# Kernel tuning notes

Hardware: AMD Instinct MI355X
Metric: run time of the kernel (lower is better)

Reference implementation:

```python
import jax, jax.numpy as jnp
import numpy as np

J = 24  # fixed pooling window (SampleLength/N = 1200/50)


def setup_inputs() -> dict:
    key = jax.random.key(0)
    k1, k2, k3 = jax.random.split(key, 3)
    T, N, K, C = 786432, 50, 400, 10  # T = 32768 segments * J
    x = jax.random.normal(k1, (T, N), dtype=jnp.float32)
    W1 = jax.random.normal(k2, (K, N), dtype=jnp.float32) * 0.1
    W2 = jax.random.normal(k3, (C, K), dtype=jnp.float32) * 0.1
    return {"x": x, "W1": W1, "W2": W2}


def reference(x, W1, W2):
    # linear + relu: [T, N] @ [N, K] -> [T, K]
    local_features = jax.nn.relu(jnp.einsum('tn,kn->tk', x, W1))
    # fixed-window mean over consecutive J rows: [T, K] -> [T//J, K]
    T, K = local_features.shape
    features = local_features.reshape(T // J, J, K).mean(axis=1)
    # final linear: [T//J, K] @ [K, C] -> [T//J, C]
    logits = jnp.einsum('bk,ck->bc', features, W2)
    return logits
```

## Files before the change

### kernel.cpp

```cpp
#include <hip/hip_runtime.h>
#include <hip/hip_bf16.h>

#define T_TOTAL 786432
#define N_IN 50
#define K_FEAT 400
#define C_OUT 10
#define NSEG 32768

#define W1F_TASKS (25 * 2 * 64)
#define W2T_OFF_BYTES 51200
#define W2T_FLOATS (25 * 320)
#define W1F32_OFF_BYTES 98304
#define W1F32_TASKS (13 * 4 * 64)
#define W2P_OFF_BYTES 163840
#define W2P_TASKS (13 * 32)
#define PREP_TASKS (W1F_TASKS + W2T_FLOATS + W1F32_TASKS + W2P_TASKS)
#define WS_NEEDED (W2P_OFF_BYTES + (size_t)W2P_TASKS * 12 * 4)

typedef __bf16 bfx8 __attribute__((ext_vector_type(8)));
typedef short  s16x8 __attribute__((ext_vector_type(8)));
typedef float  f32x2 __attribute__((ext_vector_type(2)));
typedef float  f32x4 __attribute__((ext_vector_type(4)));
typedef float  f32x16 __attribute__((ext_vector_type(16)));

static __device__ __forceinline__ short f2bf(float f) {
    union { float f; unsigned u; } v; v.f = f;
    unsigned r = v.u + 0x7fffu + ((v.u >> 16) & 1u);
    return (short)(r >> 16);
}

__global__ void prep_kernel(const float* __restrict__ W1,
                            const float* __restrict__ W2,
                            short* __restrict__ w1f, float* __restrict__ w2t,
                            short* __restrict__ w1f32, float* __restrict__ w2p)
{
    const int gid = blockIdx.x * blockDim.x + threadIdx.x;
    if (gid < W1F_TASKS) {
        const int lane = gid & 63;
        const int s    = (gid >> 6) & 1;
        const int tile = gid >> 7;
        const int m16  = lane & 15;
        const int quad = lane >> 4;
        const float* row = W1 + (tile * 16 + m16) * N_IN;
        s16x8 v;
        #pragma unroll
        for (int j = 0; j < 8; ++j) {
            const int n = s * 32 + quad * 8 + j;
            v[j] = (n < N_IN) ? f2bf(row[n]) : (short)0;
        }
        *(s16x8*)&w1f[gid * 8] = v;
    } else if (gid < W1F_TASKS + W2T_FLOATS) {
        const int i   = gid - W1F_TASKS;
        const int j   = i / 320;
        const int tid = i - j * 320;
        const int o    = tid >> 4;
        const int part = tid & 15;
        const int seg  = (o >= 10) ? 1 : 0;
        const int cls  = o - seg * 10;
        w2t[i] = W2[cls * K_FEAT + part * 25 + j];
    } else if (gid < W1F_TASKS + W2T_FLOATS + W1F32_TASKS) {
        const int i    = gid - W1F_TASKS - W2T_FLOATS;
        const int lane = i & 63;
        const int fi   = i >> 6;
        const int ft   = fi >> 2;
        const int kt   = fi & 3;
        const int feat = ft * 32 + (lane & 31);
        const int cbase = kt * 16 + (lane >> 5) * 8;
        s16x8 v;
        #pragma unroll
        for (int j = 0; j < 8; ++j) {
            const int col = cbase + j;
            v[j] = (feat < K_FEAT && col < N_IN) ? f2bf(W1[feat * N_IN + col])
                                                 : (short)0;
        }
        *(s16x8*)&w1f32[i * 8] = v;
    } else if (gid < PREP_TASKS) {
        const int i    = gid - W1F_TASKS - W2T_FLOATS - W1F32_TASKS;
        const int ft   = i >> 5;
        const int m32  = i & 31;
        const int feat = 32 * ft + m32;
        float v[12];
        #pragma unroll
        for (int c = 0; c < 12; ++c)
            v[c] = (c < C_OUT && feat < K_FEAT) ? W2[c * K_FEAT + feat] : 0.f;
        float4* dst = (float4*)&w2p[(size_t)i * 12];
        dst[0] = make_float4(v[0], v[1], v[2], v[3]);
        dst[1] = make_float4(v[4], v[5], v[6], v[7]);
        dst[2] = make_float4(v[8], v[9], v[10], v[11]);
    }
}

__global__ __launch_bounds__(256, 3) void phase1_kernel(
    const float* __restrict__ x, const short* __restrict__ w1f32,
    const float* __restrict__ w2p, float* __restrict__ out)
{
    __shared__ __align__(16) short xs[4 * 4800];
    const int tid  = threadIdx.x;
    const int lane = tid & 63;
    const int wv   = tid >> 6;
    const int m32  = lane & 31;
    const int h    = lane >> 5;
    const int chunk = blockIdx.x * 4 + wv;
    short* myxs = xs + wv * 4800;
    const s16x8* wf = (const s16x8*)w1f32;

    auto loadB = [&](s16x8* B, int ft) {
        #pragma unroll
        for (int kt = 0; kt < 4; ++kt) B[kt] = wf[(ft * 4 + kt) * 64 + lane];
    };

    s16x8 Bc[4];
    loadB(Bc, 0);

    {
        const float* xg = x + (size_t)chunk * 4800;
        #pragma unroll
        for (int i = 0; i < 19; ++i) {
            const int q = 64 * i + lane;
            if (i < 18 || lane < 48) {
                const float4 v = *(const float4*)(xg + 4 * q);
                int lo, hi;
                asm("v_cvt_pk_bf16_f32 %0, %1, %2" : "=v"(lo) : "v"(v.x), "v"(v.y));
                asm("v_cvt_pk_bf16_f32 %0, %1, %2" : "=v"(hi) : "v"(v.z), "v"(v.w));
                int2 pk; pk.x = lo; pk.y = hi;
                *(int2*)&myxs[4 * q] = pk;
            }
        }
    }
    asm volatile("s_waitcnt lgkmcnt(0)" ::: "memory");
    __builtin_amdgcn_sched_barrier(0);

    s16x8 Af[3][4];
    #pragma unroll
    for (int rt = 0; rt < 3; ++rt) {
        const int row = 32 * rt + m32;
        const short* rp = myxs + row * 50 + 8 * h;
        #pragma unroll
        for (int kt = 0; kt < 3; ++kt) {
            int d0 = *(const int*)(rp + 16 * kt + 0);
            int d1 = *(const int*)(rp + 16 * kt + 2);
            int d2 = *(const int*)(rp + 16 * kt + 4);
            int d3 = *(const int*)(rp + 16 * kt + 6);
            int4 di = {d0, d1, d2, d3};
            Af[rt][kt] = __builtin_bit_cast(s16x8, di);
        }
        int dt = 0;
        if (h == 0) dt = *(const int*)(myxs + row * 50 + 48);
        int4 di3 = {dt, 0, 0, 0};
        Af[rt][3] = __builtin_bit_cast(s16x8, di3);
    }

    const int segbase = chunk * 4;

    f32x2 oacc[4][5];
    #pragma unroll
    for (int s = 0; s < 4; ++s)
        #pragma unroll
        for (int k = 0; k < 5; ++k) { oacc[s][k][0] = 0.f; oacc[s][k][1] = 0.f; }

    const f32x2 z2 = {0.f, 0.f};

    for (int ft = 0; ft < 13; ++ft) {
        const float* wl = w2p + (size_t)(ft * 32 + m32) * 12;
        const float4 wa = *(const float4*)wl;
        const float4 wb = *(const float4*)(wl + 4);
        const float2 wc2 = *(const float2*)(wl + 8);

        float s0 = 0.f, s1 = 0.f, s2 = 0.f, s3 = 0.f;
        #pragma unroll
        for (int rt = 0; rt < 3; ++rt) {
            f32x16 acc;
            #pragma unroll
            for (int r = 0; r < 16; ++r) acc[r] = 0.f;
            __builtin_amdgcn_s_setprio(1);
            #pragma unroll
            for (int kt = 0; kt < 4; ++kt)
                acc = __builtin_amdgcn_mfma_f32_32x32x16_bf16(
                        __builtin_bit_cast(bfx8, Af[rt][kt]),
                        __builtin_bit_cast(bfx8, Bc[kt]), acc, 0, 0, 0);
            __builtin_amdgcn_s_setprio(0);
            f32x2 cv0 = z2, cv1 = z2;
            #pragma unroll
            for (int p = 0; p < 8; ++p) {
                f32x2 v2; v2[0] = acc[2 * p]; v2[1] = acc[2 * p + 1];
                v2 = __builtin_elementwise_max(v2, z2);
                if ((p >> 1) < 3 - rt) cv0 += v2; else cv1 += v2;
            }
            const float c0 = cv0[0] + cv0[1];
            const float c1 = cv1[0] + cv1[1];
            if (rt == 0)      { s0 += c0; s1 += c1; }
            else if (rt == 1) { s1 += c0; s2 += c1; }
            else              { s2 += c0; s3 += c1; }
        }
        if (ft < 12) loadB(Bc, ft + 1);

        f32x2 wp[5];
        wp[0][0] = wa.x; wp[0][1] = wa.y;
        wp[1][0] = wa.z; wp[1][1] = wa.w;
        wp[2][0] = wb.x; wp[2][1] = wb.y;
        wp[3][0] = wb.z; wp[3][1] = wb.w;
        wp[4][0] = wc2.x; wp[4][1] = wc2.y;
        const f32x2 sv0 = {s0, s0}, sv1 = {s1, s1}, sv2 = {s2, s2}, sv3 = {s3, s3};
        #pragma unroll
        for (int k = 0; k < 5; ++k) {
            oacc[0][k] = __builtin_elementwise_fma(sv0, wp[k], oacc[0][k]);
            oacc[1][k] = __builtin_elementwise_fma(sv1, wp[k], oacc[1][k]);
            oacc[2][k] = __builtin_elementwise_fma(sv2, wp[k], oacc[2][k]);
            oacc[3][k] = __builtin_elementwise_fma(sv3, wp[k], oacc[3][k]);
        }
    }

    #pragma unroll
    for (int s = 0; s < 4; ++s)
        #pragma unroll
        for (int k = 0; k < 5; ++k)
            #pragma unroll
            for (int p = 0; p < 2; ++p) {
                float v = oacc[s][k][p];
                v += __shfl_xor(v, 1);
                v += __shfl_xor(v, 2);
                v += __shfl_xor(v, 4);
                v += __shfl_xor(v, 8);
                v += __shfl_xor(v, 16);
                v += __shfl_xor(v, 32);
                oacc[s][k][p] = v;
            }
    if (lane == 0) {
        #pragma unroll
        for (int s = 0; s < 4; ++s)
            #pragma unroll
            for (int k = 0; k < 5; ++k)
                #pragma unroll
                for (int p = 0; p < 2; ++p)
                    out[(size_t)(segbase + s) * C_OUT + 2 * k + p] =
                        oacc[s][k][p] * (1.0f / 24.0f);
    }
}

#define FB_CPB 4
#define FB_NTHREADS 320
#define FB_XS_STRIDE 72
#define FB_XS_ROWS (FB_CPB * 48)

__global__ __launch_bounds__(FB_NTHREADS) void classifier_fb(
    const float* __restrict__ x, const short* __restrict__ w1f,
    const float* __restrict__ w2t, float* __restrict__ out)
{
    __shared__ short xs[FB_XS_ROWS * FB_XS_STRIDE];
    __shared__ float pooled[2 * K_FEAT];

    const int tid  = threadIdx.x;
    const int wave = tid >> 6;
    const int lane = tid & 63;
    const int m16  = lane & 15;
    const int quad = lane >> 4;

    {
        const float* xb = x + (size_t)blockIdx.x * (FB_XS_ROWS * N_IN);
        #pragma unroll
        for (int it = 0; it < (FB_XS_ROWS * 25) / FB_NTHREADS; ++it) {
            const int i = tid + it * FB_NTHREADS;
            const int r = i / 25;
            const int c2 = i - r * 25;
            const float2 v = *(const float2*)(xb + 2 * i);
            const int packed = (unsigned short)f2bf(v.x) |
                               ((unsigned)(unsigned short)f2bf(v.y) << 16);
            *(int*)&xs[r * FB_XS_STRIDE + 2 * c2] = packed;
        }
        for (int i = tid; i < FB_XS_ROWS * 7; i += FB_NTHREADS) {
            const int r = i / 7;
            const int c = 50 + 2 * (i - r * 7);
            *(int*)&xs[r * FB_XS_STRIDE + c] = 0;
        }
    }

    s16x8 bfrag[5][2];
    {
        const s16x8* wf = (const s16x8*)w1f;
        #pragma unroll
        for (int t = 0; t < 5; ++t)
            #pragma unroll
            for (int s = 0; s < 2; ++s)
                bfrag[t][s] = wf[((wave * 5 + t) * 2 + s) * 64 + lane];
    }

    const int o    = tid >> 4;
    const int part = tid & 15;
    const int segO = (o >= 10) ? 1 : 0;
    const int cls  = o - segO * 10;
    float w2r[25];
    #pragma unroll
    for (int j = 0; j < 25; ++j) w2r[j] = w2t[j * FB_NTHREADS + tid];

    __syncthreads();

    for (int ciq = 0; ciq < FB_CPB; ++ciq) {
        s16x8 a[3][2];
        #pragma unroll
        for (int r = 0; r < 3; ++r) {
            const short* arow =
                &xs[(ciq * 48 + r * 16 + m16) * FB_XS_STRIDE + quad * 8];
            a[r][0] = *(const s16x8*)(arow);
            a[r][1] = *(const s16x8*)(arow + 32);
        }
        #pragma unroll
        for (int t = 0; t < 5; ++t) {
            float c0 = 0.f, c1 = 0.f;
            #pragma unroll
            for (int r = 0; r < 3; ++r) {
                f32x4 acc = {0.f, 0.f, 0.f, 0.f};
                acc = __builtin_amdgcn_mfma_f32_16x16x32_bf16(
                        __builtin_bit_cast(bfx8, a[r][0]),
                        __builtin_bit_cast(bfx8, bfrag[t][0]), acc, 0, 0, 0);
                acc = __builtin_amdgcn_mfma_f32_16x16x32_bf16(
                        __builtin_bit_cast(bfx8, a[r][1]),
                        __builtin_bit_cast(bfx8, bfrag[t][1]), acc, 0, 0, 0);
                const float s = fmaxf(acc[0], 0.f) + fmaxf(acc[1], 0.f)
                              + fmaxf(acc[2], 0.f) + fmaxf(acc[3], 0.f);
                if (r * 4 + quad < 6) c0 += s; else c1 += s;
            }
            c0 += __shfl_xor(c0, 16); c0 += __shfl_xor(c0, 32);
            c1 += __shfl_xor(c1, 16); c1 += __shfl_xor(c1, 32);
            if (quad == 0) {
                const int feat = (wave * 5 + t) * 16 + m16;
                pooled[feat] = c0;
                pooled[K_FEAT + feat] = c1;
            }
        }
        __syncthreads();

        float sum = 0.f;
        const float* pv = &pooled[segO * K_FEAT + part * 25];
        #pragma unroll
        for (int j = 0; j < 25; ++j) sum += pv[j] * w2r[j];
        sum += __shfl_down(sum, 8, 16);
        sum += __shfl_down(sum, 4, 16);
        sum += __shfl_down(sum, 2, 16);
        sum += __shfl_down(sum, 1, 16);
        if (part == 0) {
            const int chunk = blockIdx.x * FB_CPB + ciq;
            out[(chunk * 2 + segO) * C_OUT + cls] = sum * (1.0f / 24.0f);
        }
        __syncthreads();
    }
}

extern "C" void kernel_launch(void* const* d_in, const int* in_sizes, int n_in,
                              void* d_out, int out_size, void* d_ws, size_t ws_size,
                              hipStream_t stream) {
    const float* x  = (const float*)d_in[0];
    const float* W1 = (const float*)d_in[1];
    const float* W2 = (const float*)d_in[2];
    float* out = (float*)d_out;

    short* w1f   = (short*)d_ws;
    float* w2t   = (float*)((char*)d_ws + W2T_OFF_BYTES);
    short* w1f32 = (short*)((char*)d_ws + W1F32_OFF_BYTES);
    float* w2p   = (float*)((char*)d_ws + W2P_OFF_BYTES);

    prep_kernel<<<(PREP_TASKS + 255) / 256, 256, 0, stream>>>(W1, W2, w1f, w2t,
                                                              w1f32, w2p);

    if (ws_size >= WS_NEEDED) {
        phase1_kernel<<<2048, 256, 0, stream>>>(x, w1f32, w2p, out);
    } else {
        classifier_fb<<<4096, FB_NTHREADS, 0, stream>>>(x, w1f, w2t, out);
    }
}
```

Before: 255.1 us.

## Split each 96-row chunk across three waves with shared-memory partial reduction

Previously one wave handled a whole 4-segment chunk (3 row tiles of 32). Now each block handles one chunk with three waves, each taking one 32-row tile, and the per-wave segment partials are combined through shared memory before writing. This cuts per-wave register use and serial work and allows higher occupancy (5 blocks per SIMD hint) with 4x more blocks. It adds block-level syncs and redundant B-weight loads per wave (each wave reloads the full W1 fragments).

```diff
diff --git a/kernel.cpp b/kernel.cpp
--- a/kernel.cpp
+++ b/kernel.cpp
@@ -90,18 +90,18 @@
     }
 }
 
-__global__ __launch_bounds__(256, 3) void phase1_kernel(
+__global__ __launch_bounds__(192, 5) void phase1_rt(
     const float* __restrict__ x, const short* __restrict__ w1f32,
     const float* __restrict__ w2p, float* __restrict__ out)
 {
-    __shared__ __align__(16) short xs[4 * 4800];
+    __shared__ __align__(16) short xs[4800];
+    __shared__ float part[3][20];
     const int tid  = threadIdx.x;
     const int lane = tid & 63;
     const int wv   = tid >> 6;
     const int m32  = lane & 31;
     const int h    = lane >> 5;
-    const int chunk = blockIdx.x * 4 + wv;
-    short* myxs = xs + wv * 4800;
+    const int chunk = blockIdx.x;
     const s16x8* wf = (const s16x8*)w1f32;
 
     auto loadB = [&](s16x8* B, int ft) {
@@ -115,26 +115,24 @@
     {
         const float* xg = x + (size_t)chunk * 4800;
         #pragma unroll
-        for (int i = 0; i < 19; ++i) {
-            const int q = 64 * i + lane;
-            if (i < 18 || lane < 48) {
+        for (int i = 0; i < 7; ++i) {
+            const int q = 192 * i + tid;
+            if (i < 6 || tid < 48) {
                 const float4 v = *(const float4*)(xg + 4 * q);
                 int lo, hi;
                 asm("v_cvt_pk_bf16_f32 %0, %1, %2" : "=v"(lo) : "v"(v.x), "v"(v.y));
                 asm("v_cvt_pk_bf16_f32 %0, %1, %2" : "=v"(hi) : "v"(v.z), "v"(v.w));
                 int2 pk; pk.x = lo; pk.y = hi;
-                *(int2*)&myxs[4 * q] = pk;
+                *(int2*)&xs[4 * q] = pk;
             }
         }
     }
-    asm volatile("s_waitcnt lgkmcnt(0)" ::: "memory");
-    __builtin_amdgcn_sched_barrier(0);
-
-    s16x8 Af[3][4];
-    #pragma unroll
-    for (int rt = 0; rt < 3; ++rt) {
-        const int row = 32 * rt + m32;
-        const short* rp = myxs + row * 50 + 8 * h;
+    __syncthreads();
+
+    s16x8 Af[4];
+    {
+        const int row = 32 * wv + m32;
+        const short* rp = xs + row * 50 + 8 * h;
         #pragma unroll
         for (int kt = 0; kt < 3; ++kt) {
             int d0 = *(const int*)(rp + 16 * kt + 0);
@@ -142,19 +140,17 @@
             int d2 = *(const int*)(rp + 16 * kt + 4);
             int d3 = *(const int*)(rp + 16 * kt + 6);
             int4 di = {d0, d1, d2, d3};
-            Af[rt][kt] = __builtin_bit_cast(s16x8, di);
+            Af[kt] = __builtin_bit_cast(s16x8, di);
         }
         int dt = 0;
-        if (h == 0) dt = *(const int*)(myxs + row * 50 + 48);
+        if (h == 0) dt = *(const int*)(xs + row * 50 + 48);
         int4 di3 = {dt, 0, 0, 0};
-        Af[rt][3] = __builtin_bit_cast(s16x8, di3);
-    }
-
-    const int segbase = chunk * 4;
-
-    f32x2 oacc[4][5];
+        Af[3] = __builtin_bit_cast(s16x8, di3);
+    }
+
+    f32x2 oacc[2][5];
     #pragma unroll
-    for (int s = 0; s < 4; ++s)
+    for (int s = 0; s < 2; ++s)
         #pragma unroll
         for (int k = 0; k < 5; ++k) { oacc[s][k][0] = 0.f; oacc[s][k][1] = 0.f; }
 
@@ -166,33 +162,32 @@
         const float4 wb = *(const float4*)(wl + 4);
         const float2 wc2 = *(const float2*)(wl + 8);
 
-        float s0 = 0.f, s1 = 0.f, s2 = 0.f, s3 = 0.f;
-        #pragma unroll
-        for (int rt = 0; rt < 3; ++rt) {
-            f32x16 acc;
-            #pragma unroll
-            for (int r = 0; r < 16; ++r) acc[r] = 0.f;
-            __builtin_amdgcn_s_setprio(1);
-            #pragma unroll
-            for (int kt = 0; kt < 4; ++kt)
-                acc = __builtin_amdgcn_mfma_f32_32x32x16_bf16(
-                        __builtin_bit_cast(bfx8, Af[rt][kt]),
-                        __builtin_bit_cast(bfx8, Bc[kt]), acc, 0, 0, 0);
-            __builtin_amdgcn_s_setprio(0);
-            f32x2 cv0 = z2, cv1 = z2;
-            #pragma unroll
-            for (int p = 0; p < 8; ++p) {
-                f32x2 v2; v2[0] = acc[2 * p]; v2[1] = acc[2 * p + 1];
-                v2 = __builtin_elementwise_max(v2, z2);
-                if ((p >> 1) < 3 - rt) cv0 += v2; else cv1 += v2;
-            }
-            const float c0 = cv0[0] + cv0[1];
-            const float c1 = cv1[0] + cv1[1];
-            if (rt == 0)      { s0 += c0; s1 += c1; }
-            else if (rt == 1) { s1 += c0; s2 += c1; }
-            else              { s2 += c0; s3 += c1; }
-        }
+        f32x16 acc;
+        #pragma unroll
+        for (int r = 0; r < 16; ++r) acc[r] = 0.f;
+        __builtin_amdgcn_s_setprio(1);
+        #pragma unroll
+        for (int kt = 0; kt < 4; ++kt)
+            acc = __builtin_amdgcn_mfma_f32_32x32x16_bf16(
+                    __builtin_bit_cast(bfx8, Af[kt]),
+                    __builtin_bit_cast(bfx8, Bc[kt]), acc, 0, 0, 0);
+        __builtin_amdgcn_s_setprio(0);
         if (ft < 12) loadB(Bc, ft + 1);
+
+        f32x2 gs[4];
+        #pragma unroll
+        for (int g = 0; g < 4; ++g) {
+            f32x2 a0; a0[0] = acc[4 * g + 0]; a0[1] = acc[4 * g + 1];
+            f32x2 a1; a1[0] = acc[4 * g + 2]; a1[1] = acc[4 * g + 3];
+            gs[g] = __builtin_elementwise_max(a0, z2)
+                  + __builtin_elementwise_max(a1, z2);
+        }
+        f32x2 cv0, cv1;
+        if (wv == 0)      { cv0 = gs[0] + gs[1] + gs[2]; cv1 = gs[3]; }
+        else if (wv == 1) { cv0 = gs[0] + gs[1];         cv1 = gs[2] + gs[3]; }
+        else              { cv0 = gs[0];                 cv1 = gs[1] + gs[2] + gs[3]; }
+        const float c0 = cv0[0] + cv0[1];
+        const float c1 = cv1[0] + cv1[1];
 
         f32x2 wp[5];
         wp[0][0] = wa.x; wp[0][1] = wa.y;
@@ -200,18 +195,16 @@
         wp[2][0] = wb.x; wp[2][1] = wb.y;
         wp[3][0] = wb.z; wp[3][1] = wb.w;
         wp[4][0] = wc2.x; wp[4][1] = wc2.y;
-        const f32x2 sv0 = {s0, s0}, sv1 = {s1, s1}, sv2 = {s2, s2}, sv3 = {s3, s3};
+        const f32x2 c0v = {c0, c0}, c1v = {c1, c1};
         #pragma unroll
         for (int k = 0; k < 5; ++k) {
-            oacc[0][k] = __builtin_elementwise_fma(sv0, wp[k], oacc[0][k]);
-            oacc[1][k] = __builtin_elementwise_fma(sv1, wp[k], oacc[1][k]);
-            oacc[2][k] = __builtin_elementwise_fma(sv2, wp[k], oacc[2][k]);
-            oacc[3][k] = __builtin_elementwise_fma(sv3, wp[k], oacc[3][k]);
+            oacc[0][k] = __builtin_elementwise_fma(c0v, wp[k], oacc[0][k]);
+            oacc[1][k] = __builtin_elementwise_fma(c1v, wp[k], oacc[1][k]);
         }
     }
 
     #pragma unroll
-    for (int s = 0; s < 4; ++s)
+    for (int s = 0; s < 2; ++s)
         #pragma unroll
         for (int k = 0; k < 5; ++k)
             #pragma unroll
@@ -227,13 +220,22 @@
             }
     if (lane == 0) {
         #pragma unroll
-        for (int s = 0; s < 4; ++s)
+        for (int s = 0; s < 2; ++s)
             #pragma unroll
             for (int k = 0; k < 5; ++k)
                 #pragma unroll
                 for (int p = 0; p < 2; ++p)
-                    out[(size_t)(segbase + s) * C_OUT + 2 * k + p] =
-                        oacc[s][k][p] * (1.0f / 24.0f);
+                    part[wv][s * 10 + 2 * k + p] = oacc[s][k][p];
+    }
+    __syncthreads();
+
+    if (tid < 40) {
+        const int s = tid / 10;
+        const int c = tid - s * 10;
+        float v = 0.f;
+        if (s < 3) v += part[s][c];
+        if (s > 0) v += part[s - 1][10 + c];
+        out[(size_t)(chunk * 4 + s) * C_OUT + c] = v * (1.0f / 24.0f);
     }
 }
 
@@ -362,7 +364,7 @@
                                                               w1f32, w2p);
 
     if (ws_size >= WS_NEEDED) {
-        phase1_kernel<<<2048, 256, 0, stream>>>(x, w1f32, w2p, out);
+        phase1_rt<<<8192, 192, 0, stream>>>(x, w1f32, w2p, out);
     } else {
         classifier_fb<<<4096, FB_NTHREADS, 0, stream>>>(x, w1f, w2t, out);
     }
```

Result: slower. 282.4 us (+10.7%).
